# Performance work log

Measured on AMD Instinct MI355X. Metric: run time of the kernel, lower is better.

The kernel has to match this reference:

```python
import jax, jax.numpy as jnp
import numpy as np

N_NODES = 50000
N_EDGES = 800000
IN_DIM = 2
EDGE_DIM = 2
HIDDEN = 64
N_LAYERS = 3
MAX_LEAKS = 3


def setup_inputs() -> dict:
    key = jax.random.key(0)
    ks = iter(jax.random.split(key, 32))
    s = 0.05
    inp = {
        "x": jax.random.normal(next(ks), (N_NODES, IN_DIM), dtype=jnp.float32),
        "edge_index": jax.random.randint(next(ks), (2, N_EDGES), 0, N_NODES, dtype=jnp.int32),
        "edge_attr": jax.random.normal(next(ks), (N_EDGES, EDGE_DIM), dtype=jnp.float32),
        # input projection
        "W_in": jax.random.normal(next(ks), (IN_DIM, HIDDEN), dtype=jnp.float32) * s,
        "b_in": jnp.zeros((HIDDEN,), jnp.float32),
        # message-passing layers (stacked over L)
        "W_msg": jax.random.normal(next(ks), (N_LAYERS, HIDDEN + EDGE_DIM, HIDDEN), dtype=jnp.float32) * s,
        "b_msg": jnp.zeros((N_LAYERS, HIDDEN), jnp.float32),
        "W_upd": jax.random.normal(next(ks), (N_LAYERS, 2 * HIDDEN, HIDDEN), dtype=jnp.float32) * s,
        "b_upd": jnp.zeros((N_LAYERS, HIDDEN), jnp.float32),
        # per-node leak-logit head
        "W_node": jax.random.normal(next(ks), (HIDDEN, 1), dtype=jnp.float32) * s,
        "b_node": jnp.zeros((1,), jnp.float32),
        # global no-leak head
        "W_pool": jax.random.normal(next(ks), (HIDDEN, 1), dtype=jnp.float32) * s,
        "b_pool": jnp.zeros((1,), jnp.float32),
        # num_leaks head: Linear(H, H//2) -> ReLU -> Linear(H//2, max_leaks+1)
        "W_h1": jax.random.normal(next(ks), (HIDDEN, HIDDEN // 2), dtype=jnp.float32) * s,
        "b_h1": jnp.zeros((HIDDEN // 2,), jnp.float32),
        "W_h2": jax.random.normal(next(ks), (HIDDEN // 2, MAX_LEAKS + 1), dtype=jnp.float32) * s,
        "b_h2": jnp.zeros((MAX_LEAKS + 1,), jnp.float32),
    }
    return inp


def _run_gnn(x, src, dst, edge_attr, W_in, b_in, W_msg, b_msg, W_upd, b_upd):
    """input_proj + num_layers of message passing; returns node embeddings h [N, H]."""
    n_nodes = x.shape[0]
    h = x @ W_in + b_in  # [N, H]
    # in-degree for mean aggregation (clamped to avoid div-by-zero)
    deg = jax.ops.segment_sum(jnp.ones((src.shape[0],), h.dtype), dst, num_segments=n_nodes)
    deg = jnp.maximum(deg, 1.0)[:, None]  # [N, 1]
    for l in range(N_LAYERS):
        # message: MLP over [h_src || edge_attr], gathered along edges
        m = jax.nn.relu(jnp.concatenate([h[src], edge_attr], axis=-1) @ W_msg[l] + b_msg[l])  # [E, H]
        agg = jax.ops.segment_sum(m, dst, num_segments=n_nodes) / deg  # [N, H]
        # update: MLP over [h || agg]
        h = jax.nn.relu(jnp.concatenate([h, agg], axis=-1) @ W_upd[l] + b_upd[l])  # [N, H]
    return h


def reference(x, edge_index, edge_attr, W_in, b_in, W_msg, b_msg, W_upd, b_upd,
              W_node, b_node, W_pool, b_pool, W_h1, b_h1, W_h2, b_h2):
    src, dst = edge_index[0], edge_index[1]
    # base GNN forward (dropout is identity at inference)
    h = _run_gnn(x, src, dst, edge_attr, W_in, b_in, W_msg, b_msg, W_upd, b_upd)  # [N, H]
    node_logits = (h @ W_node + b_node)[:, 0]          # [N]
    node_probs = jax.nn.sigmoid(node_logits)           # [N]
    # the multi-leak forward re-runs input_proj + mp_layers; identical math -> reuse h
    h_global = jnp.mean(h, axis=0, keepdims=True)      # [1, H]
    num_leaks_logits = jax.nn.relu(h_global @ W_h1 + b_h1) @ W_h2 + b_h2  # [1, max_leaks+1]
    return node_probs, num_leaks_logits, h
```

## Files before the change

### kernel.cpp

```cpp
#include <hip/hip_runtime.h>
#include <math.h>

constexpr int H = 64;

typedef __attribute__((ext_vector_type(8))) short bf16x8;
typedef __attribute__((ext_vector_type(4))) float f32x4;
typedef unsigned long long u64;

__device__ inline unsigned short f2bf(float f) {
  union { float f; unsigned int u; } c; c.f = f;
  unsigned int u = c.u;
  return (unsigned short)((u + 0x7FFF + ((u >> 16) & 1)) >> 16);
}
__device__ inline float bf2f(unsigned int s) {
  union { unsigned int u; float f; } c; c.u = s << 16;
  return c.f;
}
__device__ inline unsigned char f2fp8(float f) {
  return (unsigned char)(__builtin_amdgcn_cvt_pk_fp8_f32(f, f, 0, false) & 0xFF);
}

__global__ void k_prep(int* __restrict__ hist, float* __restrict__ hsumP,
                       int* __restrict__ bcur2,
                       const float* __restrict__ Wmsg, const float* __restrict__ Wupd,
                       unsigned short* __restrict__ WmT, unsigned short* __restrict__ WuT,
                       int n) {
  int t = blockIdx.x * blockDim.x + threadIdx.x;
  if (t < n) hist[t] = 0;
  if (t < 512) hsumP[t] = 0.f;
  if (t < 64) bcur2[t] = 0;
  int u = t - n;
  if (u >= 0 && u < 3 * 12288) {
    int l = u / 12288, rem = u % 12288;
    if (rem < 4096) {
      int j = rem >> 6, k = rem & 63;
      WmT[l * 4096 + rem] = f2bf(Wmsg[(size_t)l * 66 * 64 + k * 64 + j]);
    } else {
      int r2 = rem - 4096;
      int j = r2 >> 7, k = r2 & 127;
      WuT[l * 8192 + r2] = f2bf(Wupd[(size_t)l * 128 * 64 + k * 64 + j]);
    }
  }
}

__global__ void k_hist(const int* __restrict__ dst, int* __restrict__ hist, int E) {
  int e = blockIdx.x * blockDim.x + threadIdx.x;
  if (e < E) atomicAdd(&hist[dst[e]], 1);
}

__global__ void k_scan1(const int* __restrict__ hist, int* __restrict__ bsum, int n) {
  __shared__ int sred[256];
  int tid = threadIdx.x;
  int base = blockIdx.x * 1024 + tid * 4;
  int s = 0;
#pragma unroll
  for (int k = 0; k < 4; ++k) { int i = base + k; if (i < n) s += hist[i]; }
  sred[tid] = s;
  __syncthreads();
  for (int d = 128; d > 0; d >>= 1) {
    if (tid < d) sred[tid] += sred[tid + d];
    __syncthreads();
  }
  if (tid == 0) bsum[blockIdx.x] = sred[0];
}

__global__ void k_scan2(int* __restrict__ bsum, int nb) {
  __shared__ int sd[1024];
  int tid = threadIdx.x;
  int v = (tid < nb) ? bsum[tid] : 0;
  sd[tid] = v;
  __syncthreads();
  for (int d = 1; d < 1024; d <<= 1) {
    int t = (tid >= d) ? sd[tid - d] : 0;
    __syncthreads();
    sd[tid] += t;
    __syncthreads();
  }
  if (tid < nb) bsum[tid] = sd[tid] - v;
}

__global__ void k_scan3(const int* __restrict__ hist, const int* __restrict__ bsum,
                        int* __restrict__ row_ptr, int* __restrict__ pos, int n) {
  __shared__ int sth[256];
  int tid = threadIdx.x;
  int base = blockIdx.x * 1024 + tid * 4;
  int v[4]; int s = 0;
#pragma unroll
  for (int k = 0; k < 4; ++k) { int i = base + k; v[k] = (i < n) ? hist[i] : 0; s += v[k]; }
  sth[tid] = s;
  __syncthreads();
  for (int d = 1; d < 256; d <<= 1) {
    int t = (tid >= d) ? sth[tid - d] : 0;
    __syncthreads();
    sth[tid] += t;
    __syncthreads();
  }
  int run = bsum[blockIdx.x] + sth[tid] - s;
  if (blockIdx.x == 0 && tid == 0) row_ptr[0] = 0;
#pragma unroll
  for (int k = 0; k < 4; ++k) {
    int i = base + k;
    if (i < n) {
      pos[i] = run;
      run += v[k];
      row_ptr[i + 1] = run;
    }
  }
}

__global__ void k_part(const int* __restrict__ src, const int* __restrict__ dst,
                       const float2* __restrict__ ea2,
                       int* __restrict__ hist, int* __restrict__ bcur2,
                       u64* __restrict__ staged, int E, int B, int C) {
  __shared__ u64 srt[2048];
  __shared__ int cnt[64], offs[64], gbase[64];
  int tid = threadIdx.x;
  int base = blockIdx.x * 2048;
  if (tid < 64) cnt[tid] = 0;
  __syncthreads();
  u64 rec_[8]; int bk_[8], rk_[8];
#pragma unroll
  for (int k = 0; k < 8; ++k) {
    int e = base + k * 256 + tid;
    if (e < E) {
      int d = dst[e];
      atomicAdd(&hist[d], 1);
      int bk = d >> 10;
      float2 eav = ea2[e];
      unsigned int eap = (unsigned int)f2bf(eav.x) | ((unsigned int)f2bf(eav.y) << 16);
      rec_[k] = (u64)(unsigned int)(src[e] & 0xFFFF)
              | ((u64)(unsigned int)(d & 1023) << 16)
              | ((u64)(unsigned int)bk << 26)
              | ((u64)eap << 32);
      bk_[k] = bk;
      rk_[k] = atomicAdd(&cnt[bk], 1);
    } else bk_[k] = -1;
  }
  __syncthreads();
  if (tid == 0) {
    int run = 0;
    for (int b = 0; b < B; ++b) { offs[b] = run; run += cnt[b]; }
  }
  __syncthreads();
#pragma unroll
  for (int k = 0; k < 8; ++k)
    if (bk_[k] >= 0) srt[offs[bk_[k]] + rk_[k]] = rec_[k];
  __syncthreads();
  if (tid < B && cnt[tid] > 0) gbase[tid] = atomicAdd(&bcur2[tid], cnt[tid]);
  __syncthreads();
  int total = (base + 2048 <= E) ? 2048 : (E > base ? E - base : 0);
  for (int i = tid; i < total; i += 256) {
    u64 r = srt[i];
    int bk = (int)((r >> 26) & 63u);
    staged[(size_t)bk * C + gbase[bk] + (i - offs[bk])] = r;
  }
}

__global__ void k_place(const u64* __restrict__ staged, const int* __restrict__ bcur2,
                        const int* __restrict__ rptr,
                        u64* __restrict__ erec, int N_, int C) {
  __shared__ int cnt2[1024];
  __shared__ int rptrL[1025];
  int b = blockIdx.x;
  int nd0 = b << 10;
  int nn = min(nd0 + 1024, N_) - nd0;
  int tid = threadIdx.x;
  if (tid < nn) { cnt2[tid] = 0; rptrL[tid] = rptr[nd0 + tid]; }
  if (tid == 0) rptrL[nn] = rptr[nd0 + nn];
  __syncthreads();
  int count = bcur2[b];
  const u64* sb = staged + (size_t)b * C;
  for (int i = tid; i < count; i += 1024) {
    u64 r = sb[i];
    int dl = (int)((r >> 16) & 1023u);
    int p = rptrL[dl] + atomicAdd(&cnt2[dl], 1);
    erec[p] = (r & 0xFFFFull) | ((r >> 32) << 32);
  }
}

__global__ void k_scatter(const int* __restrict__ src, const int* __restrict__ dst,
                          const float* __restrict__ ea, int* __restrict__ pos,
                          u64* __restrict__ erec, int E) {
  int e = blockIdx.x * blockDim.x + threadIdx.x;
  if (e < E) {
    int d = dst[e];
    int p = atomicAdd(&pos[d], 1);
    u64 lo = f2bf(ea[2 * e]);
    u64 hi = f2bf(ea[2 * e + 1]);
    erec[p] = (u64)(unsigned int)src[e] | ((lo | (hi << 16)) << 32);
  }
}

__global__ void k_inproj_gemm(const float* __restrict__ x, const float* __restrict__ Win,
                              const float* __restrict__ bin,
                              const unsigned short* __restrict__ wmt,
                              unsigned short* __restrict__ hb,
                              unsigned char* __restrict__ g, int n) {
  int lane = threadIdx.x & 63;
  int wv = blockIdx.x * (blockDim.x >> 6) + (threadIdx.x >> 6);
  int v0 = wv * 16;
  if (v0 >= n) return;
  int r16 = lane & 15, hi = lane >> 4;
  int row = v0 + r16;
  float x0 = 0.f, x1 = 0.f;
  if (row < n) { x0 = x[2 * row]; x1 = x[2 * row + 1]; }
  union { bf16x8 v; unsigned short u[8]; } af[2];
#pragma unroll
  for (int s = 0; s < 2; ++s)
#pragma unroll
    for (int t = 0; t < 8; ++t) {
      int j = s * 32 + hi * 8 + t;
      af[s].u[t] = f2bf(fmaf(x0, Win[j], fmaf(x1, Win[64 + j], bin[j])));
    }
  if (row < n) {
    *(bf16x8*)(hb + (size_t)row * H + hi * 8)      = af[0].v;
    *(bf16x8*)(hb + (size_t)row * H + 32 + hi * 8) = af[1].v;
  }
  bf16x8 bfr[2][4];
#pragma unroll
  for (int ks = 0; ks < 2; ++ks)
#pragma unroll
    for (int jt = 0; jt < 4; ++jt)
      bfr[ks][jt] = *(const bf16x8*)(wmt + (jt * 16 + r16) * 64 + ks * 32 + hi * 8);
  f32x4 acc[4] = {};
#pragma unroll
  for (int ks = 0; ks < 2; ++ks)
#pragma unroll
    for (int jt = 0; jt < 4; ++jt)
      acc[jt] = __builtin_amdgcn_mfma_f32_16x16x32_bf16(af[ks].v, bfr[ks][jt], acc[jt], 0, 0, 0);
#pragma unroll
  for (int jt = 0; jt < 4; ++jt) {
    int col = jt * 16 + r16;
#pragma unroll
    for (int r = 0; r < 4; ++r) {
      int orow = v0 + hi * 4 + r;
      if (orow < n) g[(size_t)orow * H + col] = f2fp8(acc[jt][r]);
    }
  }
}

__device__ inline void acc8(float* a, uint2 gw, float e0, float e1,
                            const float4 waL, const float4 waH,
                            const float4 wbL, const float4 wbH,
                            const float4 bL, const float4 bH) {
  a[0] += fmaxf(fmaf(e0, waL.x, fmaf(e1, wbL.x, __builtin_amdgcn_cvt_f32_fp8(gw.x, 0) + bL.x)), 0.f);
  a[1] += fmaxf(fmaf(e0, waL.y, fmaf(e1, wbL.y, __builtin_amdgcn_cvt_f32_fp8(gw.x, 1) + bL.y)), 0.f);
  a[2] += fmaxf(fmaf(e0, waL.z, fmaf(e1, wbL.z, __builtin_amdgcn_cvt_f32_fp8(gw.x, 2) + bL.z)), 0.f);
  a[3] += fmaxf(fmaf(e0, waL.w, fmaf(e1, wbL.w, __builtin_amdgcn_cvt_f32_fp8(gw.x, 3) + bL.w)), 0.f);
  a[4] += fmaxf(fmaf(e0, waH.x, fmaf(e1, wbH.x, __builtin_amdgcn_cvt_f32_fp8(gw.y, 0) + bH.x)), 0.f);
  a[5] += fmaxf(fmaf(e0, waH.y, fmaf(e1, wbH.y, __builtin_amdgcn_cvt_f32_fp8(gw.y, 1) + bH.y)), 0.f);
  a[6] += fmaxf(fmaf(e0, waH.z, fmaf(e1, wbH.z, __builtin_amdgcn_cvt_f32_fp8(gw.y, 2) + bH.z)), 0.f);
  a[7] += fmaxf(fmaf(e0, waH.w, fmaf(e1, wbH.w, __builtin_amdgcn_cvt_f32_fp8(gw.y, 3) + bH.w)), 0.f);
}

__global__ void k_layer(const unsigned char* __restrict__ g_in,
                        const int* __restrict__ row_ptr, const u64* __restrict__ erec,
                        const float* __restrict__ Wm2, const float* __restrict__ bm,
                        unsigned short* __restrict__ hb,
                        const unsigned short* __restrict__ wut,
                        const float* __restrict__ bu,
                        const unsigned short* __restrict__ wmt_next,
                        unsigned char* __restrict__ g_out,
                        float* __restrict__ hout,
                        const float* __restrict__ Wn, const float* __restrict__ bn,
                        float* __restrict__ probs, float* __restrict__ hsumP,
                        int n) {
  __shared__ __align__(16) unsigned short aggL[32][72];
  __shared__ __align__(16) unsigned short hstage[2][16][72];
  __shared__ float shsum[64];
  int v0 = blockIdx.x * 32;

  {
    int gid = threadIdx.x >> 3, r = threadIdx.x & 7;
    int j0 = r * 8;
    float4 waL = *(const float4*)(Wm2 + j0);
    float4 waH = *(const float4*)(Wm2 + j0 + 4);
    float4 wbL = *(const float4*)(Wm2 + 64 + j0);
    float4 wbH = *(const float4*)(Wm2 + 64 + j0 + 4);
    float4 bL  = *(const float4*)(bm + j0);
    float4 bH  = *(const float4*)(bm + j0 + 4);
    int v = v0 + gid;
    uint4 o = make_uint4(0, 0, 0, 0);
    if (v < n) {
      int beg = row_ptr[v], end = row_ptr[v + 1];
      float a[8] = {0.f, 0.f, 0.f, 0.f, 0.f, 0.f, 0.f, 0.f};
      int i = beg;
      for (; i + 3 < end; i += 4) {
        u64 rA = erec[i], rB = erec[i + 1], rC = erec[i + 2], rD = erec[i + 3];
        uint2 gwA = *(const uint2*)(g_in + (size_t)(unsigned int)rA * H + j0);
        uint2 gwB = *(const uint2*)(g_in + (size_t)(unsigned int)rB * H + j0);
        uint2 gwC = *(const uint2*)(g_in + (size_t)(unsigned int)rC * H + j0);
        uint2 gwD = *(const uint2*)(g_in + (size_t)(unsigned int)rD * H + j0);
        unsigned int eA = (unsigned int)(rA >> 32), eB = (unsigned int)(rB >> 32);
        unsigned int eC = (unsigned int)(rC >> 32), eD = (unsigned int)(rD >> 32);
        acc8(a, gwA, bf2f(eA & 0xffffu), bf2f(eA >> 16), waL, waH, wbL, wbH, bL, bH);
        acc8(a, gwB, bf2f(eB & 0xffffu), bf2f(eB >> 16), waL, waH, wbL, wbH, bL, bH);
        acc8(a, gwC, bf2f(eC & 0xffffu), bf2f(eC >> 16), waL, waH, wbL, wbH, bL, bH);
        acc8(a, gwD, bf2f(eD & 0xffffu), bf2f(eD >> 16), waL, waH, wbL, wbH, bL, bH);
      }
      for (; i < end; ++i) {
        u64 rA = erec[i];
        uint2 gwA = *(const uint2*)(g_in + (size_t)(unsigned int)rA * H + j0);
        unsigned int eA = (unsigned int)(rA >> 32);
        acc8(a, gwA, bf2f(eA & 0xffffu), bf2f(eA >> 16), waL, waH, wbL, wbH, bL, bH);
      }
      float inv = 1.f / fmaxf((float)(end - beg), 1.f);
      o.x = (unsigned int)f2bf(a[0] * inv) | ((unsigned int)f2bf(a[1] * inv) << 16);
      o.y = (unsigned int)f2bf(a[2] * inv) | ((unsigned int)f2bf(a[3] * inv) << 16);
      o.z = (unsigned int)f2bf(a[4] * inv) | ((unsigned int)f2bf(a[5] * inv) << 16);
      o.w = (unsigned int)f2bf(a[6] * inv) | ((unsigned int)f2bf(a[7] * inv) << 16);
    }
    *(uint4*)(&aggL[gid][j0]) = o;
  }
  __syncthreads();

  int lane = threadIdx.x & 63;
  int w = threadIdx.x >> 6;
  bool mw = (w < 2);
  int wv0 = v0 + w * 16;
  bool act = mw && (wv0 < n);
  int r16 = lane & 15, hi = lane >> 4;
  if (hout && threadIdx.x < 64) shsum[threadIdx.x] = 0.f;
  bf16x8 bfr[4][4];
#pragma unroll
  for (int ks = 0; ks < 4; ++ks)
#pragma unroll
    for (int jt = 0; jt < 4; ++jt)
      bfr[ks][jt] = *(const bf16x8*)(wut + (jt * 16 + r16) * 128 + ks * 32 + hi * 8);
  f32x4 acc[4];
#pragma unroll
  for (int jt = 0; jt < 4; ++jt) {
    float b = bu[jt * 16 + r16];
    acc[jt] = (f32x4){b, b, b, b};
  }
  bf16x8 afr[4];
  int row = wv0 + r16;
  if (act && row < n) {
    const unsigned short* hrow = hb + (size_t)row * H + hi * 8;
    afr[0] = *(const bf16x8*)(hrow);
    afr[1] = *(const bf16x8*)(hrow + 32);
  } else {
    afr[0] = afr[1] = (bf16x8){0,0,0,0,0,0,0,0};
  }
  if (mw) {
    int lw = w * 16 + r16;
    afr[2] = *(const bf16x8*)(&aggL[lw][hi * 8]);
    afr[3] = *(const bf16x8*)(&aggL[lw][32 + hi * 8]);
  } else {
    afr[2] = afr[3] = (bf16x8){0,0,0,0,0,0,0,0};
  }
#pragma unroll
  for (int ks = 0; ks < 4; ++ks)
#pragma unroll
    for (int jt = 0; jt < 4; ++jt)
      acc[jt] = __builtin_amdgcn_mfma_f32_16x16x32_bf16(afr[ks], bfr[ks][jt], acc[jt], 0, 0, 0);
  float ov[4][4];
  unsigned short ob[4][4];
#pragma unroll
  for (int jt = 0; jt < 4; ++jt) {
    int col = jt * 16 + r16;
#pragma unroll
    for (int r = 0; r < 4; ++r) {
      int orow = wv0 + hi * 4 + r;
      bool ok = act && orow < n;
      float o = fmaxf(acc[jt][r], 0.f);
      ov[jt][r] = ok ? o : 0.f;
      ob[jt][r] = f2bf(ov[jt][r]);
      if (ok) {
        hb[(size_t)orow * H + col] = ob[jt][r];
        if (hout) hout[(size_t)orow * H + col] = o;
      }
    }
  }
  if (wmt_next) {
    if (mw) {
#pragma unroll
      for (int jt = 0; jt < 4; ++jt)
#pragma unroll
        for (int r = 0; r < 4; ++r)
          hstage[w][hi * 4 + r][jt * 16 + r16] = ob[jt][r];
    }
    __syncthreads();
    if (mw) {
      bf16x8 af2[2];
      af2[0] = *(const bf16x8*)(&hstage[w][r16][hi * 8]);
      af2[1] = *(const bf16x8*)(&hstage[w][r16][32 + hi * 8]);
      bf16x8 bf2r[2][4];
#pragma unroll
      for (int ks = 0; ks < 2; ++ks)
#pragma unroll
        for (int jt = 0; jt < 4; ++jt)
          bf2r[ks][jt] = *(const bf16x8*)(wmt_next + (jt * 16 + r16) * 64 + ks * 32 + hi * 8);
      f32x4 acc2[4] = {};
#pragma unroll
      for (int ks = 0; ks < 2; ++ks)
#pragma unroll
        for (int jt = 0; jt < 4; ++jt)
          acc2[jt] = __builtin_amdgcn_mfma_f32_16x16x32_bf16(af2[ks], bf2r[ks][jt], acc2[jt], 0, 0, 0);
#pragma unroll
      for (int jt = 0; jt < 4; ++jt) {
        int col = jt * 16 + r16;
#pragma unroll
        for (int r = 0; r < 4; ++r) {
          int orow = wv0 + hi * 4 + r;
          if (act && orow < n) g_out[(size_t)orow * H + col] = f2fp8(acc2[jt][r]);
        }
      }
    }
  } else {
    float bn0 = bn[0];
    float lg[4] = {0.f, 0.f, 0.f, 0.f};
#pragma unroll
    for (int jt = 0; jt < 4; ++jt) {
      float wn = Wn[jt * 16 + r16];
#pragma unroll
      for (int r = 0; r < 4; ++r) lg[r] = fmaf(ov[jt][r], wn, lg[r]);
    }
#pragma unroll
    for (int d = 1; d < 16; d <<= 1) {
#pragma unroll
      for (int r = 0; r < 4; ++r) lg[r] += __shfl_xor(lg[r], d);
    }
    if (r16 == 0 && act) {
#pragma unroll
      for (int r = 0; r < 4; ++r) {
        int orow = wv0 + hi * 4 + r;
        if (orow < n) probs[orow] = 1.f / (1.f + expf(-(lg[r] + bn0)));
      }
    }
    __syncthreads();
#pragma unroll
    for (int jt = 0; jt < 4; ++jt) {
      float s = ov[jt][0] + ov[jt][1] + ov[jt][2] + ov[jt][3];
      s += __shfl_xor(s, 16); s += __shfl_xor(s, 32);
      if (hi == 0) atomicAdd(&shsum[jt * 16 + r16], s);
    }
    __syncthreads();
    if (threadIdx.x < 64)
      atomicAdd(&hsumP[((blockIdx.x & 7) << 6) + threadIdx.x], shsum[threadIdx.x]);
  }
}

__global__ void k_final(const float* __restrict__ hsumP,
                        const float* __restrict__ W1, const float* __restrict__ b1,
                        const float* __restrict__ W2, const float* __restrict__ b2,
                        float* __restrict__ out4, float n_nodes) {
  __shared__ float hmean[64];
  __shared__ float z1[32];
  int tid = threadIdx.x;
  if (tid < 64) {
    float s = 0.f;
#pragma unroll
    for (int b = 0; b < 8; ++b) s += hsumP[b * 64 + tid];
    hmean[tid] = s / n_nodes;
  }
  __syncthreads();
  if (tid < 32) {
    float a = b1[tid];
    for (int k = 0; k < 64; ++k) a = fmaf(hmean[k], W1[k * 32 + tid], a);
    z1[tid] = fmaxf(a, 0.f);
  }
  __syncthreads();
  if (tid < 4) {
    float a = b2[tid];
    for (int k = 0; k < 32; ++k) a = fmaf(z1[k], W2[k * 4 + tid], a);
    out4[tid] = a;
  }
}

extern "C" void kernel_launch(void* const* d_in, const int* in_sizes, int n_in,
                              void* d_out, int out_size, void* d_ws, size_t ws_size,
                              hipStream_t stream) {
  const float* x    = (const float*)d_in[0];
  const int*   ei   = (const int*)d_in[1];
  const float* ea   = (const float*)d_in[2];
  const float* Win  = (const float*)d_in[3];
  const float* bin  = (const float*)d_in[4];
  const float* Wmsg = (const float*)d_in[5];
  const float* bmsg = (const float*)d_in[6];
  const float* Wupd = (const float*)d_in[7];
  const float* bupd = (const float*)d_in[8];
  const float* Wn   = (const float*)d_in[9];
  const float* bn   = (const float*)d_in[10];
  const float* W1   = (const float*)d_in[13];
  const float* b1   = (const float*)d_in[14];
  const float* W2   = (const float*)d_in[15];
  const float* b2   = (const float*)d_in[16];

  const int N = in_sizes[0] / 2;
  const int E = in_sizes[1] / 2;
  const int* src = ei;
  const int* dst = ei + E;

  const int B = (N + 1023) >> 10;
  const int C = (2 * (E / (B > 0 ? B : 1)) + 2048 + 255) & ~255;

  char* ws = (char*)d_ws;
  size_t off = 0;
  auto alloc = [&](size_t bytes) {
    void* p = ws + off;
    off = (off + bytes + 255) & ~(size_t)255;
    return p;
  };
  int*   hist  = (int*)  alloc((size_t)N * 4);
  int*   rptr  = (int*)  alloc((size_t)(N + 1) * 4);
  int*   pos   = (int*)  alloc((size_t)N * 4);
  int*   bsum  = (int*)  alloc((size_t)1024 * 4);
  int*   bcur2 = (int*)  alloc((size_t)64 * 4);
  u64*   staged = (u64*) alloc((size_t)(B <= 64 ? 64 : 0) * C * 8 + 8);
  u64*   erec  = (u64*)  alloc((size_t)E * 8);
  unsigned short* hb   = (unsigned short*)alloc((size_t)N * H * 2);
  unsigned char*  gA   = (unsigned char*) alloc((size_t)N * H);
  unsigned char*  gB   = (unsigned char*) alloc((size_t)N * H);
  unsigned short* WmT  = (unsigned short*)alloc((size_t)3 * 64 * 64 * 2);
  unsigned short* WuT  = (unsigned short*)alloc((size_t)3 * 64 * 128 * 2);
  float* hsumP = (float*)alloc(8 * 64 * 4);
  (void)ws_size;

  float* probs = (float*)d_out;
  float* out4  = probs + N;
  float* h     = out4 + 4;

  int eb = (E + 255) / 256;
  int sb = (N + 1023) / 1024;
  k_prep<<<(N + 3 * 12288 + 255) / 256, 256, 0, stream>>>(hist, hsumP, bcur2,
                                                          Wmsg, Wupd, WmT, WuT, N);
  if (B <= 64) {
    k_part<<<(E + 2047) / 2048, 256, 0, stream>>>(src, dst, (const float2*)ea,
                                                  hist, bcur2, staged, E, B, C);
    k_scan1<<<sb, 256, 0, stream>>>(hist, bsum, N);
    k_scan2<<<1, 1024, 0, stream>>>(bsum, sb);
    k_scan3<<<sb, 256, 0, stream>>>(hist, bsum, rptr, pos, N);
    k_place<<<B, 1024, 0, stream>>>(staged, bcur2, rptr, erec, N, C);
  } else {
    k_hist<<<eb, 256, 0, stream>>>(dst, hist, E);
    k_scan1<<<sb, 256, 0, stream>>>(hist, bsum, N);
    k_scan2<<<1, 1024, 0, stream>>>(bsum, sb);
    k_scan3<<<sb, 256, 0, stream>>>(hist, bsum, rptr, pos, N);
    k_scatter<<<eb, 256, 0, stream>>>(src, dst, ea, pos, erec, E);
  }

  int tiles = (N + 15) / 16;
  int mb = (tiles + 3) / 4;
  k_inproj_gemm<<<mb, 256, 0, stream>>>(x, Win, bin, WmT, hb, gA, N);

  int lb = (N + 31) / 32;
  for (int l = 0; l < 3; ++l) {
    const unsigned char* gin = (l & 1) ? gB : gA;
    unsigned char* gout      = (l & 1) ? gA : gB;
    k_layer<<<lb, 256, 0, stream>>>(gin, rptr, erec,
                                    Wmsg + (size_t)l * 66 * 64 + 64 * 64,
                                    bmsg + (size_t)l * 64,
                                    hb, WuT + (size_t)l * 64 * 128,
                                    bupd + (size_t)l * 64,
                                    (l < 2) ? (WmT + (size_t)(l + 1) * 64 * 64) : nullptr,
                                    gout,
                                    (l == 2) ? h : nullptr,
                                    Wn, bn, probs, hsumP, N);
  }

  k_final<<<1, 64, 0, stream>>>(hsumP, W1, b1, W2, b2, out4, (float)N);
}
```

Before: 214.9 us.

## Shrink partition chunks, parallel-scan bucket offsets, and split placement across more blocks

The partition kernel now handles 512 edges per block instead of 2048, so many more blocks are launched. The serial single-thread bucket offset loop becomes a wavefront shuffle scan, and the global base reservation is merged into that step, removing one barrier. The placement kernel is split into KP=8 blocks per bucket and uses global atomics on the per-node pos cursors instead of shared-memory counters. This raises parallelism in the CSR build, which previously used only about 49 blocks for placement, at the cost of global atomic contention and less coalesced staged writes.

```diff
diff --git a/kernel.cpp b/kernel.cpp
--- a/kernel.cpp
+++ b/kernel.cpp
@@ -112,15 +112,15 @@
                        const float2* __restrict__ ea2,
                        int* __restrict__ hist, int* __restrict__ bcur2,
                        u64* __restrict__ staged, int E, int B, int C) {
-  __shared__ u64 srt[2048];
+  __shared__ u64 srt[512];
   __shared__ int cnt[64], offs[64], gbase[64];
   int tid = threadIdx.x;
-  int base = blockIdx.x * 2048;
+  int base = blockIdx.x * 512;
   if (tid < 64) cnt[tid] = 0;
   __syncthreads();
-  u64 rec_[8]; int bk_[8], rk_[8];
-#pragma unroll
-  for (int k = 0; k < 8; ++k) {
+  u64 rec_[2]; int bk_[2], rk_[2];
+#pragma unroll
+  for (int k = 0; k < 2; ++k) {
     int e = base + k * 256 + tid;
     if (e < E) {
       int d = dst[e];
@@ -137,18 +137,23 @@
     } else bk_[k] = -1;
   }
   __syncthreads();
-  if (tid == 0) {
-    int run = 0;
-    for (int b = 0; b < B; ++b) { offs[b] = run; run += cnt[b]; }
-  }
-  __syncthreads();
-#pragma unroll
-  for (int k = 0; k < 8; ++k)
+  if (tid < 64) {
+    int v = cnt[tid];
+    int inc = v;
+#pragma unroll
+    for (int d = 1; d < 64; d <<= 1) {
+      int t = __shfl_up(inc, d);
+      if (tid >= d) inc += t;
+    }
+    offs[tid] = inc - v;
+    if (v > 0) gbase[tid] = atomicAdd(&bcur2[tid], v);
+  }
+  __syncthreads();
+#pragma unroll
+  for (int k = 0; k < 2; ++k)
     if (bk_[k] >= 0) srt[offs[bk_[k]] + rk_[k]] = rec_[k];
   __syncthreads();
-  if (tid < B && cnt[tid] > 0) gbase[tid] = atomicAdd(&bcur2[tid], cnt[tid]);
-  __syncthreads();
-  int total = (base + 2048 <= E) ? 2048 : (E > base ? E - base : 0);
+  int total = (base + 512 <= E) ? 512 : (E > base ? E - base : 0);
   for (int i = tid; i < total; i += 256) {
     u64 r = srt[i];
     int bk = (int)((r >> 26) & 63u);
@@ -157,23 +162,20 @@
 }
 
 __global__ void k_place(const u64* __restrict__ staged, const int* __restrict__ bcur2,
-                        const int* __restrict__ rptr,
-                        u64* __restrict__ erec, int N_, int C) {
-  __shared__ int cnt2[1024];
-  __shared__ int rptrL[1025];
-  int b = blockIdx.x;
+                        int* __restrict__ pos, u64* __restrict__ erec,
+                        int C, int KP) {
+  int b = blockIdx.x / KP;
+  int j = blockIdx.x % KP;
+  int count = bcur2[b];
+  int per = (count + KP - 1) / KP;
+  int s0 = j * per;
+  int s1 = s0 + per; if (s1 > count) s1 = count;
+  const u64* sb = staged + (size_t)b * C;
   int nd0 = b << 10;
-  int nn = min(nd0 + 1024, N_) - nd0;
-  int tid = threadIdx.x;
-  if (tid < nn) { cnt2[tid] = 0; rptrL[tid] = rptr[nd0 + tid]; }
-  if (tid == 0) rptrL[nn] = rptr[nd0 + nn];
-  __syncthreads();
-  int count = bcur2[b];
-  const u64* sb = staged + (size_t)b * C;
-  for (int i = tid; i < count; i += 1024) {
+  for (int i = s0 + (int)threadIdx.x; i < s1; i += (int)blockDim.x) {
     u64 r = sb[i];
     int dl = (int)((r >> 16) & 1023u);
-    int p = rptrL[dl] + atomicAdd(&cnt2[dl], 1);
+    int p = atomicAdd(&pos[nd0 + dl], 1);
     erec[p] = (r & 0xFFFFull) | ((r >> 32) << 32);
   }
 }
@@ -526,12 +528,13 @@
   k_prep<<<(N + 3 * 12288 + 255) / 256, 256, 0, stream>>>(hist, hsumP, bcur2,
                                                           Wmsg, Wupd, WmT, WuT, N);
   if (B <= 64) {
-    k_part<<<(E + 2047) / 2048, 256, 0, stream>>>(src, dst, (const float2*)ea,
-                                                  hist, bcur2, staged, E, B, C);
+    k_part<<<(E + 511) / 512, 256, 0, stream>>>(src, dst, (const float2*)ea,
+                                                hist, bcur2, staged, E, B, C);
     k_scan1<<<sb, 256, 0, stream>>>(hist, bsum, N);
     k_scan2<<<1, 1024, 0, stream>>>(bsum, sb);
     k_scan3<<<sb, 256, 0, stream>>>(hist, bsum, rptr, pos, N);
-    k_place<<<B, 1024, 0, stream>>>(staged, bcur2, rptr, erec, N, C);
+    const int KP = 8;
+    k_place<<<B * KP, 256, 0, stream>>>(staged, bcur2, pos, erec, C, KP);
   } else {
     k_hist<<<eb, 256, 0, stream>>>(dst, hist, E);
     k_scan1<<<sb, 256, 0, stream>>>(hist, bsum, N);
```

New measurement: 255.0 us. +18.7%, slower.

## Fold degree histogram and row-pointer scan into per-bucket placement kernel

Applied to the files above, without the earlier changes.

Removes the global per-edge atomic histogram from the partition kernel and drops the three scan kernels. Each placement block now counts in-degrees for its 1024-node bucket in shared memory, runs a local prefix scan, and gets its global base by summing the preceding bucket counts. This cuts global atomics and three kernel launches on the CSR-build path. In exchange the staged records are read twice, and the bucket-base sum runs serially in one thread per block.

```diff
diff --git a/kernel.cpp b/kernel.cpp
--- a/kernel.cpp
+++ b/kernel.cpp
@@ -108,9 +108,22 @@
   }
 }
 
+__global__ void k_scatter(const int* __restrict__ src, const int* __restrict__ dst,
+                          const float* __restrict__ ea, int* __restrict__ pos,
+                          u64* __restrict__ erec, int E) {
+  int e = blockIdx.x * blockDim.x + threadIdx.x;
+  if (e < E) {
+    int d = dst[e];
+    int p = atomicAdd(&pos[d], 1);
+    u64 lo = f2bf(ea[2 * e]);
+    u64 hi = f2bf(ea[2 * e + 1]);
+    erec[p] = (u64)(unsigned int)src[e] | ((lo | (hi << 16)) << 32);
+  }
+}
+
 __global__ void k_part(const int* __restrict__ src, const int* __restrict__ dst,
                        const float2* __restrict__ ea2,
-                       int* __restrict__ hist, int* __restrict__ bcur2,
+                       int* __restrict__ bcur2,
                        u64* __restrict__ staged, int E, int B, int C) {
   __shared__ u64 srt[2048];
   __shared__ int cnt[64], offs[64], gbase[64];
@@ -124,7 +137,6 @@
     int e = base + k * 256 + tid;
     if (e < E) {
       int d = dst[e];
-      atomicAdd(&hist[d], 1);
       int bk = d >> 10;
       float2 eav = ea2[e];
       unsigned int eap = (unsigned int)f2bf(eav.x) | ((unsigned int)f2bf(eav.y) << 16);
@@ -157,37 +169,50 @@
 }
 
 __global__ void k_place(const u64* __restrict__ staged, const int* __restrict__ bcur2,
-                        const int* __restrict__ rptr,
-                        u64* __restrict__ erec, int N_, int C) {
+                        int* __restrict__ row_ptr, u64* __restrict__ erec,
+                        int N_, int C, int B) {
   __shared__ int cnt2[1024];
-  __shared__ int rptrL[1025];
+  __shared__ int rloc[1024];
+  __shared__ int sbase;
   int b = blockIdx.x;
   int nd0 = b << 10;
   int nn = min(nd0 + 1024, N_) - nd0;
   int tid = threadIdx.x;
-  if (tid < nn) { cnt2[tid] = 0; rptrL[tid] = rptr[nd0 + tid]; }
-  if (tid == 0) rptrL[nn] = rptr[nd0 + nn];
+  cnt2[tid] = 0;
+  if (tid == 0) {
+    int s = 0;
+    for (int i = 0; i < b; ++i) s += bcur2[i];
+    sbase = s;
+  }
   __syncthreads();
   int count = bcur2[b];
   const u64* sb = staged + (size_t)b * C;
   for (int i = tid; i < count; i += 1024) {
+    int dl = (int)((sb[i] >> 16) & 1023u);
+    atomicAdd(&cnt2[dl], 1);
+  }
+  __syncthreads();
+  int v = cnt2[tid];
+  rloc[tid] = v;
+  __syncthreads();
+  for (int d = 1; d < 1024; d <<= 1) {
+    int t = (tid >= d) ? rloc[tid - d] : 0;
+    __syncthreads();
+    rloc[tid] += t;
+    __syncthreads();
+  }
+  int myrp = sbase + rloc[tid] - v;
+  __syncthreads();
+  rloc[tid] = myrp;
+  cnt2[tid] = 0;
+  if (tid < nn) row_ptr[nd0 + tid] = myrp;
+  if (b == B - 1 && tid == 0) row_ptr[N_] = sbase + count;
+  __syncthreads();
+  for (int i = tid; i < count; i += 1024) {
     u64 r = sb[i];
     int dl = (int)((r >> 16) & 1023u);
-    int p = rptrL[dl] + atomicAdd(&cnt2[dl], 1);
+    int p = rloc[dl] + atomicAdd(&cnt2[dl], 1);
     erec[p] = (r & 0xFFFFull) | ((r >> 32) << 32);
-  }
-}
-
-__global__ void k_scatter(const int* __restrict__ src, const int* __restrict__ dst,
-                          const float* __restrict__ ea, int* __restrict__ pos,
-                          u64* __restrict__ erec, int E) {
-  int e = blockIdx.x * blockDim.x + threadIdx.x;
-  if (e < E) {
-    int d = dst[e];
-    int p = atomicAdd(&pos[d], 1);
-    u64 lo = f2bf(ea[2 * e]);
-    u64 hi = f2bf(ea[2 * e + 1]);
-    erec[p] = (u64)(unsigned int)src[e] | ((lo | (hi << 16)) << 32);
   }
 }
 
@@ -527,11 +552,8 @@
                                                           Wmsg, Wupd, WmT, WuT, N);
   if (B <= 64) {
     k_part<<<(E + 2047) / 2048, 256, 0, stream>>>(src, dst, (const float2*)ea,
-                                                  hist, bcur2, staged, E, B, C);
-    k_scan1<<<sb, 256, 0, stream>>>(hist, bsum, N);
-    k_scan2<<<1, 1024, 0, stream>>>(bsum, sb);
-    k_scan3<<<sb, 256, 0, stream>>>(hist, bsum, rptr, pos, N);
-    k_place<<<B, 1024, 0, stream>>>(staged, bcur2, rptr, erec, N, C);
+                                                  bcur2, staged, E, B, C);
+    k_place<<<B, 1024, 0, stream>>>(staged, bcur2, rptr, erec, N, C, B);
   } else {
     k_hist<<<eb, 256, 0, stream>>>(dst, hist, E);
     k_scan1<<<sb, 256, 0, stream>>>(hist, bsum, N);
```

Result: faster. 178.0 us (median of 2 runs) (-17.2%).
